# Kernel tuning notes

Measured on AMD Instinct MI355X. Metric: run time of the kernel, lower is better.

The kernel has to match this reference:

```python
import jax, jax.numpy as jnp
import numpy as np

EVENT_FRAC = 0.05     # event_frac passed to ingest_step
DECAY = 0.99          # baseline_ema_decay
HALF_LIFE = 256.0     # trace_half_life_steps


def setup_inputs() -> dict:
    key = jax.random.key(0)
    k0, k1, k2, k3, k4 = jax.random.split(key, 5)
    L, B, T, D, TTL = 8, 4, 2048, 1024, 1024
    return {
        'pressure': jax.random.normal(k0, (B, T), jnp.float32),
        'states': jax.random.normal(k1, (L, B, T, D), jnp.float32),
        'bank_evidence': jax.random.normal(k2, (L, TTL, D), jnp.float32),
        'baseline': jax.random.uniform(k3, (L, D), jnp.float32),
        'bank_step': jax.random.randint(k4, (L, TTL), 0, 100000).astype(jnp.int64),
        'current_step': 100000,
        'horizon_H': 64,
    }


def _future_energy(states, horizon_H):
    # states: [L,B,T,D]; mean of states^2 over window [t+1, t+horizon_H] (clipped to T)
    L, B, T, D = states.shape
    sq = states * states
    cs = jnp.concatenate([jnp.zeros_like(sq[:, :, :1]), jnp.cumsum(sq, axis=2)], axis=2)  # [L,B,T+1,D]
    t = np.arange(T)
    start = t + 1
    stop = np.minimum(t + 1 + int(horizon_H), T)
    win = jnp.take(cs, stop, axis=2) - jnp.take(cs, start, axis=2)  # [L,B,T,D] window sums
    count = jnp.asarray((stop - start).astype(np.float32))          # [T]
    fe = jnp.where(count[None, None, :, None] > 0,
                   win / jnp.maximum(count, 1.0)[None, None, :, None], 0.0)
    return fe


def reference(pressure, states, bank_evidence, baseline, bank_step, current_step, horizon_H):
    B, T = pressure.shape
    L, D = states.shape[0], states.shape[-1]
    total = B * T
    k = int(round(EVENT_FRAC * total))

    # compute_event_mask: top-k of flat pressure -> boolean mask [B,T]
    _, idx = jax.lax.top_k(pressure.reshape(-1), k)
    event_mask = jnp.zeros((total,), jnp.bool_).at[idx].set(True).reshape(B, T)

    fe = _future_energy(states, horizon_H)  # [L,B,T,D]

    # update_baseline_ema: mean future energy over non-event positions per layer/channel
    ne_f = (~event_mask).astype(jnp.float32)  # [B,T]
    obs = jnp.einsum('lbtd,bt->ld', fe, ne_f) / jnp.float32(total - k)
    new_baseline = DECAY * baseline + (1.0 - DECAY) * obs  # [L,D]

    # evidence: mean over event positions of clamp_min(fe - baseline, 0)
    ev_f = event_mask.astype(jnp.float32)
    excess = jnp.maximum(fe - new_baseline[:, None, None, :], 0.0)
    evidence = jnp.einsum('lbtd,bt->ld', excess, ev_f) / jnp.float32(k)

    # score(current_step): age-weighted bank average
    valid = (bank_step >= 0).astype(jnp.float32)  # [L,TTL]
    age = jnp.clip(current_step - bank_step, 0, None).astype(jnp.float32)
    weight = jnp.exp2(-age / HALF_LIFE) * valid
    weight_sum = weight.sum(axis=1, keepdims=True)  # [L,1]
    weighted_ev = jnp.einsum('ls,lsd->ld', weight, bank_evidence)
    score = weighted_ev / jnp.maximum(weight_sum, 1e-12)
    score = jnp.where(weight_sum > 0, score, jnp.zeros_like(score))

    return jnp.stack([evidence, new_baseline, score])  # [3,L,D]
```

## Files before the change

### kernel.cpp

```cpp
#include <hip/hip_runtime.h>
#include <cmath>
#include <climits>

#define L_    8
#define B_    4
#define T_    2048
#define D_    1024
#define TTL_  1024
#define KSLOT 512
#define EVCAP 512
#define TCQ   8
#define NCQ   (T_/TCQ)
#define GRPC  8
#define NGRP  (NCQ/GRPC)
#define TIEMAX 256
#define MAXMB 1024

__device__ __forceinline__ int waveRed(int v){
  for(int o=32;o>0;o>>=1) v += __shfl_xor(v,o,64);
  return v;
}
__device__ __forceinline__ int lowb_s(const short* a, int n, int v){
  int lo=0, hi=n;
  while(lo<hi){ int mid=(lo+hi)>>1; if((int)a[mid] < v) lo=mid+1; else hi=mid; }
  return lo;
}
__device__ __forceinline__ int uppb_s(const short* a, int n, int v){
  int lo=0, hi=n;
  while(lo<hi){ int mid=(lo+hi)>>1; if((int)a[mid] <= v) lo=mid+1; else hi=mid; }
  return lo;
}

__global__ __launch_bounds__(1024) void kA(
    const float* __restrict__ pressure, const int* __restrict__ hptr, int k,
    int* __restrict__ meta, float* __restrict__ w,
    int* __restrict__ evB, int* __restrict__ evCS, int* __restrict__ evCE,
    float* __restrict__ evInv,
    unsigned short* __restrict__ markRowG, unsigned short* __restrict__ markValG,
    int* __restrict__ mkStart, int* __restrict__ mkCnt)
{
  __shared__ unsigned ku[B_*T_];
  __shared__ short ef[B_*T_];
  __shared__ int csum[1024];
  __shared__ int cnt4[4][4];
  __shared__ int scnt;
  __shared__ int s_n[B_], s_off[B_];
  __shared__ int batchPfx[B_+1];
  __shared__ int tieIdx[TIEMAX];
  __shared__ int tieCnt;
  __shared__ short evTeSh[B_*KSLOT];
  __shared__ short evEnSh[B_*KSLOT];
  const int tid = threadIdx.x;
  const int total = B_*T_;
  const int H = hptr[0];

  for(int i=tid;i<total;i+=1024){
    union{float f;unsigned u;} v; v.f = pressure[i];
    unsigned u = v.u;
    ku[i] = (u & 0x80000000u) ? ~u : (u | 0x80000000u);
  }
  if(tid < B_) s_n[tid] = 0;
  if(tid == 0) tieCnt = 0;
  if(tid < 8) ((int*)cnt4)[tid] = 0;
  __syncthreads();

  unsigned p = 0;
  for(int it=0; it<16; ++it){
    const int bit = 30 - 2*it;
    int* A = cnt4[it&3];
    const unsigned q1 = p | (1u<<bit);
    const unsigned q2 = p | (2u<<bit);
    const unsigned q3 = p | (3u<<bit);
    int c1=0,c2=0,c3=0;
    for(int i=tid;i<total;i+=1024){
      unsigned x = ku[i];
      c1 += (x>=q1); c2 += (x>=q2); c3 += (x>=q3);
    }
    c1=waveRed(c1); c2=waveRed(c2); c3=waveRed(c3);
    if((tid&63)==0){ atomicAdd(&A[1],c1); atomicAdd(&A[2],c2); atomicAdd(&A[3],c3); }
    if(tid<4) cnt4[(it+2)&3][tid] = 0;
    __syncthreads();
    const int n1=A[1], n2=A[2], n3=A[3];
    if(n3>=k) p=q3; else if(n2>=k) p=q2; else if(n1>=k) p=q1;
  }
  __syncthreads();
  if(tid==0) scnt=0;
  __syncthreads();
  {
    int c=0;
    for(int i=tid;i<total;i+=1024) c += (ku[i] > p) ? 1 : 0;
    c = waveRed(c);
    if((tid&63)==0) atomicAdd(&scnt, c);
  }
  for(int i=tid;i<total;i+=1024){
    if(ku[i]==p){ int pos=atomicAdd(&tieCnt,1); if(pos<TIEMAX) tieIdx[pos]=i; }
  }
  __syncthreads();
  const int needed = k - scnt;

  for(int j=0;j<8;++j){
    int i = tid*8+j;
    ef[i] = (ku[i] > p) ? (short)1 : (short)0;
  }
  __syncthreads();

  if(tieCnt <= TIEMAX){
    if(tid==0){
      int cnt = tieCnt;
      for(int sel=0; sel<needed; ++sel){
        int best=INT_MAX, bi=-1;
        for(int q=0;q<cnt;++q){ int vv=tieIdx[q]; if(vv>=0 && vv<best){best=vv;bi=q;} }
        if(bi>=0){ tieIdx[bi]=-1; ef[best]=1; }
      }
    }
  } else {
    for(int j=0;j<8;++j){
      int i = tid*8+j;
      if(ku[i]==p){
        int r=0;
        for(int q=0;q<i;++q) r += (ku[q]==p) ? 1 : 0;
        if(r < needed) ef[i]=1;
      }
    }
  }
  __syncthreads();

  int own = 0;
  #pragma unroll
  for(int j=0;j<8;++j) own += ef[tid*8+j];
  csum[tid] = own;
  __syncthreads();
  for(int ofs=1; ofs<1024; ofs<<=1){
    int add = (tid>=ofs) ? csum[tid-ofs] : 0;
    __syncthreads();
    csum[tid] += add;
    __syncthreads();
  }
  if(tid < B_) batchPfx[tid] = (tid==0) ? 0 : csum[tid*256-1];
  if(tid == 0) batchPfx[B_] = csum[1023];
  __syncthreads();

  {
    const int ex = csum[tid] - own;
    int run = 0;
    for(int j=0;j<8;++j){
      int i = tid*8+j;
      if(ef[i]){
        int b = i >> 11;
        int t = i & (T_-1);
        int m = ex + run - batchPfx[b];
        if(t != T_-1){
          int c = T_-1-t; if(c>H) c=H;
          evTeSh[b*KSLOT+m] = (short)t;
          evEnSh[b*KSLOT+m] = (short)(t+c);
        }
        ++run;
      }
    }
  }
  __syncthreads();
  if(tid < B_){
    int nf = batchPfx[tid+1] - batchPfx[tid];
    nf -= (ef[tid*T_ + T_-1] ? 1 : 0);
    s_n[tid] = nf;
  }
  __syncthreads();
  if(tid==0){
    int off=0;
    for(int b=0;b<B_;++b){ meta[b]=s_n[b]; meta[4+b]=off; s_off[b]=off; off += s_n[b]; }
    meta[8] = off;
  }
  __syncthreads();

  for(int idx=tid; idx<B_*MAXMB; idx+=1024){
    const int b = idx>>10, m = idx & (MAXMB-1);
    const int n = s_n[b];
    if(m >= 2*n) continue;
    const short* S = evTeSh + b*KSLOT;
    const short* E = evEnSh + b*KSLOT;
    int rank, row, val;
    if(m < n){
      row = (int)S[m];
      rank = m + lowb_s(E, n, row);
      const int e = s_off[b] + m;
      val = e;
      const int en = (int)E[m];
      evB[e]=b; evCS[e]=row>>3; evCE[e]=en>>3;
      evInv[e] = 1.0f/(float)(en - row);
    } else {
      const int j = m - n;
      row = (int)E[j];
      rank = uppb_s(S, n, row) + j;
      val = (s_off[b] + j) | 0x8000;
    }
    markRowG[b*MAXMB+rank] = (unsigned short)row;
    markValG[b*MAXMB+rank] = (unsigned short)val;
  }

  for(int idx=tid; idx<B_*NCQ; idx+=1024){
    const int b = idx/NCQ, ch = idx%NCQ;
    const int n = s_n[b];
    const short* S = evTeSh + b*KSLOT;
    const short* E = evEnSh + b*KSLOT;
    const int lo = ch*TCQ, hi = lo+TCQ;
    const int a = lowb_s(S,n,lo) + lowb_s(E,n,lo);
    const int c = lowb_s(S,n,hi) + lowb_s(E,n,hi);
    mkStart[idx] = a; mkCnt[idx] = c - a;
  }

  for(int s=tid;s<T_;s+=1024){
    float acc = 0.f;
    int lo = s - H; if(lo < 0) lo = 0;
    for(int t2=lo; t2<s; ++t2){
      int c2 = T_-1-t2; if(c2 > H) c2 = H;
      acc += 1.0f / (float)c2;
    }
    w[s] = acc;
  }
}

__global__ __launch_bounds__(256) void kSQ(
    const float* __restrict__ states, const float* __restrict__ w,
    const int* __restrict__ mkStart, const int* __restrict__ mkCnt,
    const unsigned short* __restrict__ markRowG,
    const unsigned short* __restrict__ markValG,
    float4* __restrict__ chunkCS, float4* __restrict__ wA,
    float4* __restrict__ feS, float4* __restrict__ feE)
{
  __shared__ float lds[2][4][1024];
  __shared__ unsigned short sMr[1024];
  __shared__ unsigned short sMv[1024];
  __shared__ float sW[64];

  int bx = blockIdx.x;
  const int grp = bx & (NGRP-1); bx >>= 5;
  const int b = bx & 3; const int l = bx >> 2;
  const int tid = threadIdx.x;
  const int wv = tid >> 6, lane = tid & 63;
  const int t0 = grp * 64;
  const float* sbase = states + ((size_t)(l*B_+b)*T_ + t0)*D_;

  const int gBase = (b<<8) + grp*GRPC;
  const int mi0 = mkStart[gBase];
  const int cnt = (mkStart[gBase+GRPC-1] + mkCnt[gBase+GRPC-1]) - mi0;
  for(int i=tid; i<cnt; i+=256){
    sMr[i] = markRowG[b*MAXMB + mi0 + i];
    sMv[i] = markValG[b*MAXMB + mi0 + i];
  }
  if(tid < 64) sW[tid] = w[t0 + tid];
  __syncthreads();

  int mi = 0;
  int nextRow = (cnt > 0) ? (int)sMr[0] : INT_MAX;
  float4 R={0,0,0,0}, A={0,0,0,0};

#define ISSUE(slot_, batch_) { _Pragma("unroll") \
  for(int r_=0;r_<4;++r_){ \
    const float* g_ = sbase + (size_t)((batch_)*4 + r_)*D_ + wv*256 + lane*4; \
    __builtin_amdgcn_global_load_lds( \
        (const __attribute__((address_space(1))) void*)g_, \
        (__attribute__((address_space(3))) void*)&lds[slot_][r_][wv*256], \
        16, 0, 0); } }

  ISSUE(0,0); ISSUE(1,1);

  #pragma unroll
  for(int bb=0; bb<16; ++bb){
    if(bb < 15){ asm volatile("s_waitcnt vmcnt(4)" ::: "memory"); }
    else       { asm volatile("s_waitcnt vmcnt(0)" ::: "memory"); }
    __builtin_amdgcn_sched_barrier(0);
    const int slot = bb & 1;
    #pragma unroll
    for(int j=0;j<4;++j){
      const int t = t0 + bb*4 + j;
      float4 x = *(const float4*)&lds[slot][j][tid*4];
      float sx=x.x*x.x, sy=x.y*x.y, sz=x.z*x.z, sw=x.w*x.w;
      R.x+=sx; R.y+=sy; R.z+=sz; R.w+=sw;
      const float wj = sW[bb*4 + j];
      A.x=fmaf(wj,sx,A.x); A.y=fmaf(wj,sy,A.y);
      A.z=fmaf(wj,sz,A.z); A.w=fmaf(wj,sw,A.w);
      while(nextRow == t){
        const int me = (int)sMv[mi];
        float4* dst = (me & 0x8000) ? feE : feS;
        dst[((size_t)l*EVCAP + (me & 0x7fff))*256 + tid] = R;
        ++mi; nextRow = (mi < cnt) ? (int)sMr[mi] : INT_MAX;
      }
    }
    if(slot == 1){
      const int ch = grp*GRPC + (bb>>1);
      chunkCS[((size_t)(l*B_+b)*NCQ + ch)*256 + tid] = R;
      R.x=0.f; R.y=0.f; R.z=0.f; R.w=0.f;
    }
    asm volatile("s_waitcnt lgkmcnt(0)" ::: "memory");
    __builtin_amdgcn_sched_barrier(0);
    if(bb+2 < 16){ ISSUE(slot, bb+2); }
  }
  wA[((size_t)(l*B_+b)*NGRP + grp)*256 + tid] = A;
#undef ISSUE
}

__global__ __launch_bounds__(256) void kMid(
    const float* __restrict__ wAf, float* __restrict__ S_allP,
    const float4* __restrict__ chunkCS,
    const float4* __restrict__ feS, float4* __restrict__ feE,
    const int* __restrict__ evB, const int* __restrict__ evCS,
    const int* __restrict__ evCE, const float* __restrict__ evInv,
    const int* __restrict__ meta)
{
  if(blockIdx.x < 128){
    const int dq = blockIdx.x & 3; const int lb = blockIdx.x >> 2;
    const int d = dq*256 + threadIdx.x;
    const size_t base = (size_t)lb*NGRP*D_ + d;
    float aw = 0.f;
    #pragma unroll
    for(int g=0; g<NGRP; ++g) aw += wAf[base + (size_t)g*D_];
    S_allP[(size_t)lb*D_ + d] = aw;
  } else {
    const int bid = blockIdx.x - 128;
    const int e = bid & (EVCAP-1); const int l = bid >> 9;
    if(e >= meta[8]) return;
    const int tid = threadIdx.x;
    const int b = evB[e], cs = evCS[e], ce = evCE[e];
    const float inv = evInv[e];
    const size_t cbase = ((size_t)(l*B_+b)*NCQ)*256 + tid;
    float4 acc = {0,0,0,0};
    for(int c=cs; c<ce; ++c){
      float4 v = chunkCS[cbase + (size_t)c*256];
      acc.x+=v.x; acc.y+=v.y; acc.z+=v.z; acc.w+=v.w;
    }
    const size_t sl = ((size_t)l*EVCAP + e)*256 + tid;
    float4 Rs = feS[sl], Re = feE[sl];
    float4 fe;
    fe.x = (acc.x + Re.x - Rs.x)*inv;
    fe.y = (acc.y + Re.y - Rs.y)*inv;
    fe.z = (acc.z + Re.z - Rs.z)*inv;
    fe.w = (acc.w + Re.w - Rs.w)*inv;
    feE[sl] = fe;
  }
}

__global__ __launch_bounds__(256) void kSev(
    const float4* __restrict__ feE, const int* __restrict__ meta,
    float4* __restrict__ S_evP)
{
  const int es = blockIdx.x & 31; const int l = blockIdx.x >> 5;
  const int tid = threadIdx.x;
  const int nev = meta[8];
  const int per = (nev + 31) >> 5;
  const int e0 = es*per;
  int e1 = e0 + per; if(e1 > nev) e1 = nev;
  float4 acc = {0,0,0,0};
  for(int e=e0;e<e1;++e){
    float4 v = feE[((size_t)l*EVCAP + e)*256 + tid];
    acc.x+=v.x; acc.y+=v.y; acc.z+=v.z; acc.w+=v.w;
  }
  S_evP[((size_t)l*32 + es)*256 + tid] = acc;
}

__global__ __launch_bounds__(256) void kDS2(
    const float4* __restrict__ feE, const int* __restrict__ meta,
    const float4* __restrict__ S_allP, const float4* __restrict__ S_evP,
    const float4* __restrict__ baseline4,
    const float4* __restrict__ bank_ev4, const int* __restrict__ bank_step,
    const int* __restrict__ csptr,
    float4* __restrict__ out4, float4* __restrict__ S_exP,
    float4* __restrict__ SscoreP, int nonk)
{
  const int tid = threadIdx.x;
  if(blockIdx.x < 256){
    const int l = blockIdx.x >> 5, ech = blockIdx.x & 31;
    float4 sa = {0,0,0,0};
    #pragma unroll
    for(int b=0;b<B_;++b){
      float4 t = S_allP[((size_t)(l*B_+b))*256 + tid];
      sa.x+=t.x; sa.y+=t.y; sa.z+=t.z; sa.w+=t.w;
    }
    float4 se = {0,0,0,0};
    for(int j0=0;j0<32;j0+=8){
      float4 t[8];
      #pragma unroll
      for(int j=0;j<8;++j) t[j] = S_evP[((size_t)l*32 + j0+j)*256 + tid];
      #pragma unroll
      for(int j=0;j<8;++j){ se.x+=t[j].x; se.y+=t[j].y; se.z+=t[j].z; se.w+=t[j].w; }
    }
    const float inv_nonk = 1.0f/(float)nonk;
    const float4 bl = baseline4[(size_t)l*256 + tid];
    float4 nb;
    nb.x = 0.99f*bl.x + 0.01f*((sa.x-se.x)*inv_nonk);
    nb.y = 0.99f*bl.y + 0.01f*((sa.y-se.y)*inv_nonk);
    nb.z = 0.99f*bl.z + 0.01f*((sa.z-se.z)*inv_nonk);
    nb.w = 0.99f*bl.w + 0.01f*((sa.w-se.w)*inv_nonk);
    if(ech == 0) out4[2048 + (size_t)l*256 + tid] = nb;
    const int nev = meta[8];
    const int per = (nev + 31) >> 5;
    const int e0 = ech*per;
    int e1 = e0 + per; if(e1 > nev) e1 = nev;
    float4 acc = {0,0,0,0};
    #pragma unroll 4
    for(int e=e0;e<e1;++e){
      float4 fe = feE[((size_t)l*EVCAP + e)*256 + tid];
      acc.x += fmaxf(fe.x - nb.x, 0.f);
      acc.y += fmaxf(fe.y - nb.y, 0.f);
      acc.z += fmaxf(fe.z - nb.z, 0.f);
      acc.w += fmaxf(fe.w - nb.w, 0.f);
    }
    S_exP[((size_t)l*32 + ech)*256 + tid] = acc;
  } else {
    const int bx = blockIdx.x - 256;
    const int l = bx >> 5, sch = bx & 31;
    const int scount = TTL_/32;
    const int s0 = sch*scount;
    __shared__ float wl[TTL_/32];
    const int cs = csptr[0];
    if(tid < scount){
      int bs = bank_step[l*TTL_ + s0 + tid];
      float wgt = 0.f;
      if(bs >= 0){
        int a = cs - bs; if(a < 0) a = 0;
        wgt = exp2f(-(float)a * (1.0f/256.0f));
      }
      wl[tid] = wgt;
    }
    __syncthreads();
    float4 acc = {0,0,0,0};
    const float4* bp = bank_ev4 + ((size_t)l*TTL_ + s0)*256 + tid;
    #pragma unroll 8
    for(int j=0;j<scount;++j){
      float4 v = bp[(size_t)j*256];
      const float wv = wl[j];
      acc.x = fmaf(wv, v.x, acc.x); acc.y = fmaf(wv, v.y, acc.y);
      acc.z = fmaf(wv, v.z, acc.z); acc.w = fmaf(wv, v.w, acc.w);
    }
    SscoreP[((size_t)l*32 + sch)*256 + tid] = acc;
  }
}

__global__ __launch_bounds__(256) void kE(
    const float4* __restrict__ S_exP, const float4* __restrict__ SscoreP,
    const int* __restrict__ bank_step, const int* __restrict__ csptr,
    float4* __restrict__ out4, float kf)
{
  const int l = blockIdx.x;
  const int tid = threadIdx.x;
  __shared__ float red[256];
  const int cs = csptr[0];
  float wacc = 0.f;
  for(int s=tid; s<TTL_; s+=256){
    int bs = bank_step[l*TTL_+s];
    if(bs >= 0){
      int a = cs - bs; if(a<0) a=0;
      wacc += exp2f(-(float)a * (1.0f/256.0f));
    }
  }
  red[tid] = wacc;
  __syncthreads();
  for(int st=128; st>0; st>>=1){ if(tid<st) red[tid] += red[tid+st]; __syncthreads(); }
  const float wsum = red[0];

  float4 ex = {0,0,0,0}, ss = {0,0,0,0};
  for(int j0=0;j0<32;j0+=8){
    float4 a[8], bb[8];
    #pragma unroll
    for(int j=0;j<8;++j){
      a[j]  = S_exP[((size_t)l*32 + j0+j)*256 + tid];
      bb[j] = SscoreP[((size_t)l*32 + j0+j)*256 + tid];
    }
    #pragma unroll
    for(int j=0;j<8;++j){
      ex.x+=a[j].x; ex.y+=a[j].y; ex.z+=a[j].z; ex.w+=a[j].w;
      ss.x+=bb[j].x; ss.y+=bb[j].y; ss.z+=bb[j].z; ss.w+=bb[j].w;
    }
  }
  const float invk = 1.0f/kf;
  float4 o0 = {ex.x*invk, ex.y*invk, ex.z*invk, ex.w*invk};
  out4[(size_t)l*256 + tid] = o0;
  float4 o2 = {0,0,0,0};
  if(wsum > 0.f){
    const float wm = fmaxf(wsum, 1e-12f);
    o2.x = ss.x/wm; o2.y = ss.y/wm; o2.z = ss.z/wm; o2.w = ss.w/wm;
  }
  out4[2*2048 + (size_t)l*256 + tid] = o2;
}

extern "C" void kernel_launch(void* const* d_in, const int* in_sizes, int n_in,
                              void* d_out, int out_size, void* d_ws, size_t ws_size,
                              hipStream_t stream)
{
  const float* pressure  = (const float*)d_in[0];
  const float* states    = (const float*)d_in[1];
  const float* bank_ev   = (const float*)d_in[2];
  const float* baseline  = (const float*)d_in[3];
  const int*   bank_step = (const int*)d_in[4];
  const int*   csptr     = (const int*)d_in[5];
  const int*   hptr      = (const int*)d_in[6];
  float* out = (float*)d_out;

  const int total = B_*T_;
  const int k = (int)llround(0.05 * (double)total);

  char* ws = (char*)d_ws;
  float* w        = (float*)(ws + 0);
  int*   meta     = (int*)(ws + 8192);
  int*   evB      = (int*)(ws + 16384);
  int*   evCS     = (int*)(ws + 18432);
  int*   evCE     = (int*)(ws + 20480);
  float* evInv    = (float*)(ws + 22528);
  unsigned short* markRowG = (unsigned short*)(ws + 24576);
  unsigned short* markValG = (unsigned short*)(ws + 32768);
  int*   mkStart  = (int*)(ws + 40960);
  int*   mkCnt    = (int*)(ws + 45056);
  float* S_allP   = (float*)(ws + 65536);
  float* S_evP    = (float*)(ws + 262144);
  float* S_exP    = (float*)(ws + 1310720);
  float* SscoreP  = (float*)(ws + 2359296);
  float* chunkCS  = (float*)(ws + 4194304);
  float* wAbuf    = (float*)(ws + 37748736);
  float* feS      = (float*)(ws + 71303168);
  float* feE      = (float*)(ws + 88080384);

  const size_t need = 104857600ull;
  if(ws_size < need) return;

  kA<<<1, 1024, 0, stream>>>(pressure, hptr, k, meta, w,
                             evB, evCS, evCE, evInv,
                             markRowG, markValG, mkStart, mkCnt);
  kSQ<<<L_*B_*NGRP, 256, 0, stream>>>(states, w, mkStart, mkCnt,
                                      markRowG, markValG,
                                      (float4*)chunkCS, (float4*)wAbuf,
                                      (float4*)feS, (float4*)feE);
  kMid<<<128 + L_*EVCAP, 256, 0, stream>>>(wAbuf, S_allP,
                                           (const float4*)chunkCS,
                                           (const float4*)feS, (float4*)feE,
                                           evB, evCS, evCE, evInv, meta);
  kSev<<<L_*32, 256, 0, stream>>>((const float4*)feE, meta, (float4*)S_evP);
  kDS2<<<512, 256, 0, stream>>>((const float4*)feE, meta,
                                (const float4*)S_allP, (const float4*)S_evP,
                                (const float4*)baseline,
                                (const float4*)bank_ev, bank_step, csptr,
                                (float4*)out, (float4*)S_exP,
                                (float4*)SscoreP, total - k);
  kE<<<L_, 256, 0, stream>>>((const float4*)S_exP, (const float4*)SscoreP,
                             bank_step, csptr, (float4*)out, (float)k);
}
```

Measured before the change: 164.0 us.

## Replace per-chunk prefix sums with per-group totals and fuse event finalize with event sum

The squared-state kernel now writes one running sum per 64-row group instead of eight per-chunk partial sums. It also loads all four LDS rows before issuing the next prefetch, then does the math afterwards. Window sums for events are rebuilt from at most one group total plus the start and end snapshots, since the horizon of 64 spans at most one group boundary. The separate event-finalize and event-sum kernels are merged into one launch, which removes a kernel launch and shrinks workspace traffic. The one-boundary assumption depends on H being at most 64 and on the group size.

```diff
diff --git a/kernel.cpp b/kernel.cpp
--- a/kernel.cpp
+++ b/kernel.cpp
@@ -12,7 +12,7 @@
 #define TCQ   8
 #define NCQ   (T_/TCQ)
 #define GRPC  8
-#define NGRP  (NCQ/GRPC)
+#define NGRP  32
 #define TIEMAX 256
 #define MAXMB 1024
 
@@ -185,7 +185,7 @@
       const int e = s_off[b] + m;
       val = e;
       const int en = (int)E[m];
-      evB[e]=b; evCS[e]=row>>3; evCE[e]=en>>3;
+      evB[e]=b; evCS[e]=row>>6; evCE[e]=en>>6;
       evInv[e] = 1.0f/(float)(en - row);
     } else {
       const int j = m - n;
@@ -224,7 +224,7 @@
     const int* __restrict__ mkStart, const int* __restrict__ mkCnt,
     const unsigned short* __restrict__ markRowG,
     const unsigned short* __restrict__ markValG,
-    float4* __restrict__ chunkCS, float4* __restrict__ wA,
+    float4* __restrict__ Gbuf, float4* __restrict__ wA,
     float4* __restrict__ feS, float4* __restrict__ feE)
 {
   __shared__ float lds[2][4][1024];
@@ -262,6 +262,19 @@
         (__attribute__((address_space(3))) void*)&lds[slot_][r_][wv*256], \
         16, 0, 0); } }
 
+#define ROW(j_, xv_) { \
+    const int t = t0 + bb*4 + (j_); \
+    float sx=xv_.x*xv_.x, sy=xv_.y*xv_.y, sz=xv_.z*xv_.z, sw=xv_.w*xv_.w; \
+    R.x+=sx; R.y+=sy; R.z+=sz; R.w+=sw; \
+    const float wj = sW[bb*4 + (j_)]; \
+    A.x=fmaf(wj,sx,A.x); A.y=fmaf(wj,sy,A.y); \
+    A.z=fmaf(wj,sz,A.z); A.w=fmaf(wj,sw,A.w); \
+    while(nextRow == t){ \
+      const int me = (int)sMv[mi]; \
+      float4* dst = (me & 0x8000) ? feE : feS; \
+      dst[((size_t)l*EVCAP + (me & 0x7fff))*256 + tid] = R; \
+      ++mi; nextRow = (mi < cnt) ? (int)sMr[mi] : INT_MAX; } }
+
   ISSUE(0,0); ISSUE(1,1);
 
   #pragma unroll
@@ -270,46 +283,34 @@
     else       { asm volatile("s_waitcnt vmcnt(0)" ::: "memory"); }
     __builtin_amdgcn_sched_barrier(0);
     const int slot = bb & 1;
-    #pragma unroll
-    for(int j=0;j<4;++j){
-      const int t = t0 + bb*4 + j;
-      float4 x = *(const float4*)&lds[slot][j][tid*4];
-      float sx=x.x*x.x, sy=x.y*x.y, sz=x.z*x.z, sw=x.w*x.w;
-      R.x+=sx; R.y+=sy; R.z+=sz; R.w+=sw;
-      const float wj = sW[bb*4 + j];
-      A.x=fmaf(wj,sx,A.x); A.y=fmaf(wj,sy,A.y);
-      A.z=fmaf(wj,sz,A.z); A.w=fmaf(wj,sw,A.w);
-      while(nextRow == t){
-        const int me = (int)sMv[mi];
-        float4* dst = (me & 0x8000) ? feE : feS;
-        dst[((size_t)l*EVCAP + (me & 0x7fff))*256 + tid] = R;
-        ++mi; nextRow = (mi < cnt) ? (int)sMr[mi] : INT_MAX;
-      }
-    }
-    if(slot == 1){
-      const int ch = grp*GRPC + (bb>>1);
-      chunkCS[((size_t)(l*B_+b)*NCQ + ch)*256 + tid] = R;
-      R.x=0.f; R.y=0.f; R.z=0.f; R.w=0.f;
-    }
+    float4 x0 = *(const float4*)&lds[slot][0][tid*4];
+    float4 x1 = *(const float4*)&lds[slot][1][tid*4];
+    float4 x2 = *(const float4*)&lds[slot][2][tid*4];
+    float4 x3 = *(const float4*)&lds[slot][3][tid*4];
     asm volatile("s_waitcnt lgkmcnt(0)" ::: "memory");
     __builtin_amdgcn_sched_barrier(0);
     if(bb+2 < 16){ ISSUE(slot, bb+2); }
-  }
-  wA[((size_t)(l*B_+b)*NGRP + grp)*256 + tid] = A;
+    ROW(0,x0) ROW(1,x1) ROW(2,x2) ROW(3,x3)
+  }
+  const size_t gi = ((size_t)(l*B_+b)*NGRP + grp)*256 + tid;
+  Gbuf[gi] = R;
+  wA[gi]   = A;
 #undef ISSUE
-}
-
-__global__ __launch_bounds__(256) void kMid(
+#undef ROW
+}
+
+__global__ __launch_bounds__(256) void kFin(
     const float* __restrict__ wAf, float* __restrict__ S_allP,
-    const float4* __restrict__ chunkCS,
+    const float4* __restrict__ Gbuf,
     const float4* __restrict__ feS, float4* __restrict__ feE,
     const int* __restrict__ evB, const int* __restrict__ evCS,
     const int* __restrict__ evCE, const float* __restrict__ evInv,
-    const int* __restrict__ meta)
+    const int* __restrict__ meta, float4* __restrict__ S_evP)
 {
+  const int tid = threadIdx.x;
   if(blockIdx.x < 128){
     const int dq = blockIdx.x & 3; const int lb = blockIdx.x >> 2;
-    const int d = dq*256 + threadIdx.x;
+    const int d = dq*256 + tid;
     const size_t base = (size_t)lb*NGRP*D_ + d;
     float aw = 0.f;
     #pragma unroll
@@ -317,44 +318,31 @@
     S_allP[(size_t)lb*D_ + d] = aw;
   } else {
     const int bid = blockIdx.x - 128;
-    const int e = bid & (EVCAP-1); const int l = bid >> 9;
-    if(e >= meta[8]) return;
-    const int tid = threadIdx.x;
-    const int b = evB[e], cs = evCS[e], ce = evCE[e];
-    const float inv = evInv[e];
-    const size_t cbase = ((size_t)(l*B_+b)*NCQ)*256 + tid;
-    float4 acc = {0,0,0,0};
-    for(int c=cs; c<ce; ++c){
-      float4 v = chunkCS[cbase + (size_t)c*256];
-      acc.x+=v.x; acc.y+=v.y; acc.z+=v.z; acc.w+=v.w;
-    }
-    const size_t sl = ((size_t)l*EVCAP + e)*256 + tid;
-    float4 Rs = feS[sl], Re = feE[sl];
-    float4 fe;
-    fe.x = (acc.x + Re.x - Rs.x)*inv;
-    fe.y = (acc.y + Re.y - Rs.y)*inv;
-    fe.z = (acc.z + Re.z - Rs.z)*inv;
-    fe.w = (acc.w + Re.w - Rs.w)*inv;
-    feE[sl] = fe;
-  }
-}
-
-__global__ __launch_bounds__(256) void kSev(
-    const float4* __restrict__ feE, const int* __restrict__ meta,
-    float4* __restrict__ S_evP)
-{
-  const int es = blockIdx.x & 31; const int l = blockIdx.x >> 5;
-  const int tid = threadIdx.x;
-  const int nev = meta[8];
-  const int per = (nev + 31) >> 5;
-  const int e0 = es*per;
-  int e1 = e0 + per; if(e1 > nev) e1 = nev;
-  float4 acc = {0,0,0,0};
-  for(int e=e0;e<e1;++e){
-    float4 v = feE[((size_t)l*EVCAP + e)*256 + tid];
-    acc.x+=v.x; acc.y+=v.y; acc.z+=v.z; acc.w+=v.w;
-  }
-  S_evP[((size_t)l*32 + es)*256 + tid] = acc;
+    const int es = bid & 31; const int l = bid >> 5;
+    const int nev = meta[8];
+    const int per = (nev + 31) >> 5;
+    const int e0 = es*per;
+    int e1 = e0 + per; if(e1 > nev) e1 = nev;
+    float4 E = {0,0,0,0};
+    for(int e=e0; e<e1; ++e){
+      const int b = evB[e], gs = evCS[e], ge = evCE[e];
+      const float inv = evInv[e];
+      const size_t sl = ((size_t)l*EVCAP + e)*256 + tid;
+      float4 Rs = feS[sl], Re = feE[sl];
+      float4 fe;
+      if(gs == ge){
+        fe.x=(Re.x-Rs.x)*inv; fe.y=(Re.y-Rs.y)*inv;
+        fe.z=(Re.z-Rs.z)*inv; fe.w=(Re.w-Rs.w)*inv;
+      } else {
+        float4 G = Gbuf[((size_t)(l*B_+b)*NGRP + gs)*256 + tid];
+        fe.x=(G.x-Rs.x+Re.x)*inv; fe.y=(G.y-Rs.y+Re.y)*inv;
+        fe.z=(G.z-Rs.z+Re.z)*inv; fe.w=(G.w-Rs.w+Re.w)*inv;
+      }
+      feE[sl] = fe;
+      E.x+=fe.x; E.y+=fe.y; E.z+=fe.z; E.w+=fe.w;
+    }
+    S_evP[((size_t)l*32 + es)*256 + tid] = E;
+  }
 }
 
 __global__ __launch_bounds__(256) void kDS2(
@@ -513,12 +501,12 @@
   float* S_evP    = (float*)(ws + 262144);
   float* S_exP    = (float*)(ws + 1310720);
   float* SscoreP  = (float*)(ws + 2359296);
-  float* chunkCS  = (float*)(ws + 4194304);
-  float* wAbuf    = (float*)(ws + 37748736);
-  float* feS      = (float*)(ws + 71303168);
-  float* feE      = (float*)(ws + 88080384);
-
-  const size_t need = 104857600ull;
+  float* Gbuf     = (float*)(ws + 4194304);
+  float* wAbuf    = (float*)(ws + 8388608);
+  float* feS      = (float*)(ws + 12582912);
+  float* feE      = (float*)(ws + 29360128);
+
+  const size_t need = 46137344ull;
   if(ws_size < need) return;
 
   kA<<<1, 1024, 0, stream>>>(pressure, hptr, k, meta, w,
@@ -526,13 +514,13 @@
                              markRowG, markValG, mkStart, mkCnt);
   kSQ<<<L_*B_*NGRP, 256, 0, stream>>>(states, w, mkStart, mkCnt,
                                       markRowG, markValG,
-                                      (float4*)chunkCS, (float4*)wAbuf,
+                                      (float4*)Gbuf, (float4*)wAbuf,
                                       (float4*)feS, (float4*)feE);
-  kMid<<<128 + L_*EVCAP, 256, 0, stream>>>(wAbuf, S_allP,
-                                           (const float4*)chunkCS,
-                                           (const float4*)feS, (float4*)feE,
-                                           evB, evCS, evCE, evInv, meta);
-  kSev<<<L_*32, 256, 0, stream>>>((const float4*)feE, meta, (float4*)S_evP);
+  kFin<<<128 + 256, 256, 0, stream>>>(wAbuf, S_allP,
+                                      (const float4*)Gbuf,
+                                      (const float4*)feS, (float4*)feE,
+                                      evB, evCS, evCE, evInv, meta,
+                                      (float4*)S_evP);
   kDS2<<<512, 256, 0, stream>>>((const float4*)feE, meta,
                                 (const float4*)S_allP, (const float4*)S_evP,
                                 (const float4*)baseline,
```

New measurement: 141.6 us. 13.7% less time.
